# Kernel optimization log

Hardware: AMD Instinct MI355X
Metric: run time of the kernel (lower is better)

Reference implementation:

```python
import jax, jax.numpy as jnp
import numpy as np

TOP_K = 2
NUM_EXPERTS = 64
LOAD_BALANCE_ALPHA = 0.01
Z_LOSS_ALPHA = 1e-4
TEMPERATURE = 1.0  # buffer init, clamped to [0.1, 2.0] -> 1.0 (seq_len < 8192 branch)


def setup_inputs() -> dict:
    key = jax.random.key(0)
    k1, k2 = jax.random.split(key)
    x = jax.random.normal(k1, (4, 4096, 1024), dtype=jnp.float32)
    gate_w = jax.random.normal(k2, (NUM_EXPERTS, 1024), dtype=jnp.float32) * (1.0 / np.sqrt(1024))
    return {"x": x, "gate_w": gate_w}


def reference(x, gate_w):
    B, S, H = x.shape
    x_flat = x.reshape(-1, H)                      # [T, H], T = B*S
    logits = jnp.einsum('th,eh->te', x_flat, gate_w)  # [T, E]
    logits = logits / TEMPERATURE
    scores = jax.nn.softmax(logits, axis=-1)       # [T, E]
    # eval path: dynamic_top_k == top_k, no noise / capacity limitation
    top_scores, top_idx = jax.lax.top_k(scores, TOP_K)   # [T, K]
    top_scores = jax.nn.softmax(top_scores.astype(jnp.float32), axis=-1).astype(x.dtype)
    # load-balance loss: squared deviation of mean expert load from uniform
    expert_load = scores.mean(axis=0)              # [E]
    ideal = 1.0 / NUM_EXPERTS
    lb_loss = LOAD_BALANCE_ALPHA * NUM_EXPERTS * jnp.sum((expert_load - ideal) ** 2)
    # z-loss: mean squared logsumexp of gate logits
    z = jax.nn.logsumexp(logits, axis=-1)          # [T]
    z_loss = Z_LOSS_ALPHA * jnp.mean(z ** 2)
    total_loss = lb_loss + z_loss
    return top_scores, top_idx, total_loss
```

## Files before the change

kernel.cpp:

```cpp
#include <hip/hip_runtime.h>
#include <math.h>

#define T_TOK 16384
#define NEXP  64


__global__ void moe_prep(const float* __restrict__ gw, float* __restrict__ ws) {
    __shared__ float tile[64][65];
    const int b = blockIdx.x;
    const int tid = threadIdx.x;
    if (b == 0 && tid < 128) ws[tid] = 0.f;
#pragma unroll
    for (int it = 0; it < 16; ++it) {
        int idx = it * 256 + tid;
        int e = idx >> 6, kk = idx & 63;
        tile[e][kk] = gw[e * 1024 + b * 64 + kk];
    }
    __syncthreads();
#pragma unroll
    for (int it = 0; it < 16; ++it) {
        int idx = it * 256 + tid;
        int kk = idx >> 6, e = idx & 63;
        ws[128 + (b * 64 + kk) * 64 + e] = tile[e][kk];
    }
}

__device__ __forceinline__ void pstore(float* B, const float (&a)[8][8],
                                       int tg, int eg) {
#pragma unroll
    for (int i = 0; i < 8; ++i) {
        float* p = B + (tg + 8 * i) * 68 + (eg << 3);
        *(float4*)(p)     = make_float4(a[i][0], a[i][1], a[i][2], a[i][3]);
        *(float4*)(p + 4) = make_float4(a[i][4], a[i][5], a[i][6], a[i][7]);
    }
}
__device__ __forceinline__ void padd(float* B, const float (&a)[8][8],
                                     int tg, int eg) {
#pragma unroll
    for (int i = 0; i < 8; ++i) {
        float* p = B + (tg + 8 * i) * 68 + (eg << 3);
        float4 v0 = *(float4*)(p);
        float4 v1 = *(float4*)(p + 4);
        v0.x += a[i][0]; v0.y += a[i][1]; v0.z += a[i][2]; v0.w += a[i][3];
        v1.x += a[i][4]; v1.y += a[i][5]; v1.z += a[i][6]; v1.w += a[i][7];
        *(float4*)(p)     = v0;
        *(float4*)(p + 4) = v1;
    }
}

__launch_bounds__(1024, 4)
__global__ void moe_main(const float* __restrict__ x,
                         const float* __restrict__ wt,
                         float* __restrict__ acc_ws,
                         float* __restrict__ out) {
    __shared__ float xbuf[64 * 68];
    __shared__ float wbuf[64 * 68];
    __shared__ float sc[64 * 68];
    __shared__ float row_inv[64];
    __shared__ float colpart[16][64];
    __shared__ int   is_last;

    const int tid  = threadIdx.x;
    const int lane = tid & 63;
    const int wv   = __builtin_amdgcn_readfirstlane(tid >> 6);
    const int tg   = lane & 7;
    const int eg   = lane >> 3;
    const int tok0 = blockIdx.x << 6;

    const int rr = tid >> 4;
    const int cg = tid & 15;
    const float* gx = x + (((size_t)(tok0 + rr)) << 10) + (cg << 2);
    const float* gw = wt + (rr << 6) + (cg << 2);
    const int lof = rr * 68 + (cg << 2);

    float acc[8][8];
#pragma unroll
    for (int i = 0; i < 8; ++i)
#pragma unroll
        for (int j = 0; j < 8; ++j) acc[i][j] = 0.f;

    const float* xr = xbuf + tg * 68 + (wv << 2);
    const float* wr = wbuf + (wv * 4) * 68 + (eg << 3);

    float4 px = *(const float4*)gx;
    float4 pw = *(const float4*)gw;

#pragma unroll 1
    for (int s = 0; s < 16; ++s) {
        __syncthreads();
        *(float4*)(xbuf + lof) = px;
        *(float4*)(wbuf + lof) = pw;
        __syncthreads();
        if (s < 15) {
            px = *(const float4*)(gx + ((s + 1) << 6));
            pw = *(const float4*)(gw + ((s + 1) << 12));
        }
        float wa[4][8];
#pragma unroll
        for (int u = 0; u < 4; ++u) {
            float4 q0 = *(const float4*)(wr + u * 68);
            float4 q1 = *(const float4*)(wr + u * 68 + 4);
            wa[u][0] = q0.x; wa[u][1] = q0.y; wa[u][2] = q0.z; wa[u][3] = q0.w;
            wa[u][4] = q1.x; wa[u][5] = q1.y; wa[u][6] = q1.z; wa[u][7] = q1.w;
        }
#pragma unroll
        for (int i = 0; i < 8; ++i) {
            float4 xc = *(const float4*)(xr + i * 544);
            float xa[4] = {xc.x, xc.y, xc.z, xc.w};
#pragma unroll
            for (int u = 0; u < 4; ++u) {
                float xv = xa[u];
#pragma unroll
                for (int j = 0; j < 8; ++j)
                    acc[i][j] = fmaf(xv, wa[u][j], acc[i][j]);
            }
        }
    }

    __syncthreads();
    if      (wv == 0) pstore(sc,   acc, tg, eg);
    else if (wv == 1) pstore(xbuf, acc, tg, eg);
    else if (wv == 2) pstore(wbuf, acc, tg, eg);
    __syncthreads();
    if      (wv == 3) padd(sc,   acc, tg, eg);
    else if (wv == 4) padd(xbuf, acc, tg, eg);
    else if (wv == 5) padd(wbuf, acc, tg, eg);
    __syncthreads();
    if      (wv == 6) padd(sc,   acc, tg, eg);
    else if (wv == 7) padd(xbuf, acc, tg, eg);
    else if (wv == 8) padd(wbuf, acc, tg, eg);
    __syncthreads();
    if      (wv == 9)  padd(sc,   acc, tg, eg);
    else if (wv == 10) padd(xbuf, acc, tg, eg);
    else if (wv == 11) padd(wbuf, acc, tg, eg);
    __syncthreads();
    if      (wv == 12) padd(sc,   acc, tg, eg);
    else if (wv == 13) padd(xbuf, acc, tg, eg);
    else if (wv == 14) padd(wbuf, acc, tg, eg);
    __syncthreads();
    if (wv == 15) padd(sc, acc, tg, eg);
    __syncthreads();
    {
        const int row = tid >> 4, g = tid & 15;
        float* ps = sc + row * 68 + (g << 2);
        float4 a  = *(float4*)ps;
        float4 bx = *(const float4*)(xbuf + row * 68 + (g << 2));
        float4 bw = *(const float4*)(wbuf + row * 68 + (g << 2));
        a.x += bx.x + bw.x; a.y += bx.y + bw.y;
        a.z += bx.z + bw.z; a.w += bx.w + bw.w;
        *(float4*)ps = a;
    }
    __syncthreads();

    if (tid < 64) {
        const int r = tid;
        const float* srow = sc + r * 68;
        float v1 = -1e30f, v2 = -1e30f;
        int i1 = 0, i2 = 0;
        for (int j = 0; j < 64; ++j) {
            float l = srow[j];
            if (l > v1)      { v2 = v1; i2 = i1; v1 = l; i1 = j; }
            else if (l > v2) { v2 = l; i2 = j; }
        }
        float m = v1;
        float ssum = 0.f;
        for (int j = 0; j < 64; ++j) {
            float ev = expf(srow[j] - m);
            ssum += ev;
            sc[r * 68 + j] = ev;
        }
        float inv = 1.f / ssum;
        row_inv[r] = inv;
        float z = m + logf(ssum);
        float zsq = z * z;
#pragma unroll
        for (int off = 32; off > 0; off >>= 1) zsq += __shfl_down(zsq, off);
        if (lane == 0) atomicAdd(acc_ws + 64, zsq);

        float p1s = inv;
        float p2s = expf(v2 - m) * inv;
        float bb  = expf(p2s - p1s);
        float s1 = 1.f / (1.f + bb);
        float s2 = bb * s1;
        int t = tok0 + r;
        out[2 * t]     = s1;
        out[2 * t + 1] = s2;
        out[2 * T_TOK + 2 * t]     = (float)i1;
        out[2 * T_TOK + 2 * t + 1] = (float)i2;
    }
    __syncthreads();

    {
        int e  = tid & 63;
        int rg = tid >> 6;
        float sum = 0.f;
#pragma unroll
        for (int r2 = 0; r2 < 4; ++r2) {
            int row = (rg << 2) + r2;
            sum += sc[row * 68 + e] * row_inv[row];
        }
        colpart[rg][e] = sum;
    }
    __syncthreads();
    if (tid < 64) {
        float tot = 0.f;
#pragma unroll
        for (int rg = 0; rg < 16; ++rg) tot += colpart[rg][tid];
        atomicAdd(acc_ws + tid, tot);
    }

    __syncthreads();
    if (tid == 0) {
        __threadfence();
        int old = __hip_atomic_fetch_add((int*)(acc_ws + 66), 1,
                                         __ATOMIC_ACQ_REL, __HIP_MEMORY_SCOPE_AGENT);
        is_last = (old == 255) ? 1 : 0;
    }
    __syncthreads();
    if (is_last && tid < 64) {
        __threadfence();
        float load = __hip_atomic_load(acc_ws + tid, __ATOMIC_RELAXED,
                                       __HIP_MEMORY_SCOPE_AGENT) * (1.f / 16384.f);
        float d = load - (1.f / 64.f);
        float v = d * d;
#pragma unroll
        for (int off = 32; off > 0; off >>= 1) v += __shfl_down(v, off);
        if (tid == 0) {
            float zsum = __hip_atomic_load(acc_ws + 64, __ATOMIC_RELAXED,
                                           __HIP_MEMORY_SCOPE_AGENT);
            float lb = 0.01f * 64.f * v;
            float zl = 1e-4f * zsum * (1.f / 16384.f);
            out[4 * T_TOK] = lb + zl;
        }
    }
}

extern "C" void kernel_launch(void* const* d_in, const int* in_sizes, int n_in,
                              void* d_out, int out_size, void* d_ws, size_t ws_size,
                              hipStream_t stream) {
    const float* x  = (const float*)d_in[0];
    const float* gw = (const float*)d_in[1];
    float* out = (float*)d_out;
    float* ws  = (float*)d_ws;

    moe_prep<<<16, 256, 0, stream>>>(gw, ws);
    moe_main<<<256, 1024, 0, stream>>>(x, ws + 128, ws, out);
}
```

Baseline: 131.0 us.

## Halve block to 512 threads with 8-wave K-split and two-stage reduction

Reduces moe_main to 512 threads (8 waves), so each wave covers 8 K-columns per 64-wide chunk instead of 4, loading two float4 per thread per stage. The inner product loop is reordered to load 8 x rows once and then stream w rows, and the cross-wave partial-sum reduction shrinks from 16 waves over 3 buffers to 8 waves over 2 buffers with fewer barriers. The aim is to cut reduction and sync overhead and shared-memory traffic per FMA. The cost is half the threads per block with launch bounds allowing only one block, which may lower latency hiding while streaming x from memory.

Result: no change. 128.5 us (-1.9%).

```diff
diff --git a/kernel.cpp b/kernel.cpp
--- a/kernel.cpp
+++ b/kernel.cpp
@@ -25,20 +25,20 @@
     }
 }
 
-__device__ __forceinline__ void pstore(float* B, const float (&a)[8][8],
-                                       int tg, int eg) {
+__device__ __forceinline__ void pst88(float* B, const float (&a)[8][8],
+                                      int ta, int eb) {
 #pragma unroll
     for (int i = 0; i < 8; ++i) {
-        float* p = B + (tg + 8 * i) * 68 + (eg << 3);
+        float* p = B + (ta + (i << 3)) * 68 + (eb << 3);
         *(float4*)(p)     = make_float4(a[i][0], a[i][1], a[i][2], a[i][3]);
         *(float4*)(p + 4) = make_float4(a[i][4], a[i][5], a[i][6], a[i][7]);
     }
 }
-__device__ __forceinline__ void padd(float* B, const float (&a)[8][8],
-                                     int tg, int eg) {
+__device__ __forceinline__ void pad88(float* B, const float (&a)[8][8],
+                                      int ta, int eb) {
 #pragma unroll
     for (int i = 0; i < 8; ++i) {
-        float* p = B + (tg + 8 * i) * 68 + (eg << 3);
+        float* p = B + (ta + (i << 3)) * 68 + (eb << 3);
         float4 v0 = *(float4*)(p);
         float4 v1 = *(float4*)(p + 4);
         v0.x += a[i][0]; v0.y += a[i][1]; v0.z += a[i][2]; v0.w += a[i][3];
@@ -48,7 +48,7 @@
     }
 }
 
-__launch_bounds__(1024, 4)
+__launch_bounds__(512, 1)
 __global__ void moe_main(const float* __restrict__ x,
                          const float* __restrict__ wt,
                          float* __restrict__ acc_ws,
@@ -56,22 +56,23 @@
     __shared__ float xbuf[64 * 68];
     __shared__ float wbuf[64 * 68];
     __shared__ float sc[64 * 68];
+    __shared__ float fb[64 * 68];
     __shared__ float row_inv[64];
-    __shared__ float colpart[16][64];
+    __shared__ float colpart[8][64];
     __shared__ int   is_last;
 
     const int tid  = threadIdx.x;
     const int lane = tid & 63;
     const int wv   = __builtin_amdgcn_readfirstlane(tid >> 6);
-    const int tg   = lane & 7;
-    const int eg   = lane >> 3;
+    const int ta   = lane >> 3;
+    const int eb   = lane & 7;
     const int tok0 = blockIdx.x << 6;
 
-    const int rr = tid >> 4;
-    const int cg = tid & 15;
-    const float* gx = x + (((size_t)(tok0 + rr)) << 10) + (cg << 2);
-    const float* gw = wt + (rr << 6) + (cg << 2);
-    const int lof = rr * 68 + (cg << 2);
+    const int rr  = tid >> 3;
+    const int sub = tid & 7;
+    const float* gx = x + (((size_t)(tok0 + rr)) << 10) + (sub << 2);
+    const float* gw = wt + (rr << 6) + (sub << 2);
+    const int slo = rr * 68 + (sub << 2);
 
     float acc[8][8];
 #pragma unroll
@@ -79,76 +80,76 @@
 #pragma unroll
         for (int j = 0; j < 8; ++j) acc[i][j] = 0.f;
 
-    const float* xr = xbuf + tg * 68 + (wv << 2);
-    const float* wr = wbuf + (wv * 4) * 68 + (eg << 3);
-
-    float4 px = *(const float4*)gx;
-    float4 pw = *(const float4*)gw;
+    float4 px0 = *(const float4*)(gx);
+    float4 px1 = *(const float4*)(gx + 32);
+    float4 pw0 = *(const float4*)(gw);
+    float4 pw1 = *(const float4*)(gw + 32);
 
 #pragma unroll 1
     for (int s = 0; s < 16; ++s) {
         __syncthreads();
-        *(float4*)(xbuf + lof) = px;
-        *(float4*)(wbuf + lof) = pw;
+        *(float4*)(xbuf + slo)      = px0;
+        *(float4*)(xbuf + slo + 32) = px1;
+        *(float4*)(wbuf + slo)      = pw0;
+        *(float4*)(wbuf + slo + 32) = pw1;
         __syncthreads();
         if (s < 15) {
-            px = *(const float4*)(gx + ((s + 1) << 6));
-            pw = *(const float4*)(gw + ((s + 1) << 12));
-        }
-        float wa[4][8];
-#pragma unroll
-        for (int u = 0; u < 4; ++u) {
-            float4 q0 = *(const float4*)(wr + u * 68);
-            float4 q1 = *(const float4*)(wr + u * 68 + 4);
-            wa[u][0] = q0.x; wa[u][1] = q0.y; wa[u][2] = q0.z; wa[u][3] = q0.w;
-            wa[u][4] = q1.x; wa[u][5] = q1.y; wa[u][6] = q1.z; wa[u][7] = q1.w;
-        }
-#pragma unroll
-        for (int i = 0; i < 8; ++i) {
-            float4 xc = *(const float4*)(xr + i * 544);
-            float xa[4] = {xc.x, xc.y, xc.z, xc.w};
+            px0 = *(const float4*)(gx + ((s + 1) << 6));
+            px1 = *(const float4*)(gx + ((s + 1) << 6) + 32);
+            pw0 = *(const float4*)(gw + ((s + 1) << 12));
+            pw1 = *(const float4*)(gw + ((s + 1) << 12) + 32);
+        }
+#pragma unroll
+        for (int cc = 0; cc < 2; ++cc) {
+            const int c4 = (wv << 3) + (cc << 2);
+            float xr[8][4];
+#pragma unroll
+            for (int i = 0; i < 8; ++i) {
+                float4 v = *(const float4*)(xbuf + (ta + (i << 3)) * 68 + c4);
+                xr[i][0] = v.x; xr[i][1] = v.y; xr[i][2] = v.z; xr[i][3] = v.w;
+            }
 #pragma unroll
             for (int u = 0; u < 4; ++u) {
-                float xv = xa[u];
-#pragma unroll
-                for (int j = 0; j < 8; ++j)
-                    acc[i][j] = fmaf(xv, wa[u][j], acc[i][j]);
+                const float* wr = wbuf + (c4 + u) * 68 + (eb << 3);
+                float4 w0 = *(const float4*)(wr);
+                float4 w1 = *(const float4*)(wr + 4);
+                float wa[8] = {w0.x, w0.y, w0.z, w0.w,
+                               w1.x, w1.y, w1.z, w1.w};
+#pragma unroll
+                for (int i = 0; i < 8; ++i) {
+                    const float xs = xr[i][u];
+#pragma unroll
+                    for (int j = 0; j < 8; ++j)
+                        acc[i][j] = fmaf(xs, wa[j], acc[i][j]);
+                }
             }
         }
     }
 
-    __syncthreads();
-    if      (wv == 0) pstore(sc,   acc, tg, eg);
-    else if (wv == 1) pstore(xbuf, acc, tg, eg);
-    else if (wv == 2) pstore(wbuf, acc, tg, eg);
-    __syncthreads();
-    if      (wv == 3) padd(sc,   acc, tg, eg);
-    else if (wv == 4) padd(xbuf, acc, tg, eg);
-    else if (wv == 5) padd(wbuf, acc, tg, eg);
-    __syncthreads();
-    if      (wv == 6) padd(sc,   acc, tg, eg);
-    else if (wv == 7) padd(xbuf, acc, tg, eg);
-    else if (wv == 8) padd(wbuf, acc, tg, eg);
-    __syncthreads();
-    if      (wv == 9)  padd(sc,   acc, tg, eg);
-    else if (wv == 10) padd(xbuf, acc, tg, eg);
-    else if (wv == 11) padd(wbuf, acc, tg, eg);
-    __syncthreads();
-    if      (wv == 12) padd(sc,   acc, tg, eg);
-    else if (wv == 13) padd(xbuf, acc, tg, eg);
-    else if (wv == 14) padd(wbuf, acc, tg, eg);
-    __syncthreads();
-    if (wv == 15) padd(sc, acc, tg, eg);
+    if      (wv == 0) pst88(sc, acc, ta, eb);
+    else if (wv == 1) pst88(fb, acc, ta, eb);
+    __syncthreads();
+    if      (wv == 2) pad88(sc, acc, ta, eb);
+    else if (wv == 3) pad88(fb, acc, ta, eb);
+    __syncthreads();
+    if      (wv == 4) pad88(sc, acc, ta, eb);
+    else if (wv == 5) pad88(fb, acc, ta, eb);
+    __syncthreads();
+    if      (wv == 6) pad88(sc, acc, ta, eb);
+    else if (wv == 7) pad88(fb, acc, ta, eb);
     __syncthreads();
     {
-        const int row = tid >> 4, g = tid & 15;
+        const int row = tid >> 3, g = tid & 7;
         float* ps = sc + row * 68 + (g << 2);
-        float4 a  = *(float4*)ps;
-        float4 bx = *(const float4*)(xbuf + row * 68 + (g << 2));
-        float4 bw = *(const float4*)(wbuf + row * 68 + (g << 2));
-        a.x += bx.x + bw.x; a.y += bx.y + bw.y;
-        a.z += bx.z + bw.z; a.w += bx.w + bw.w;
-        *(float4*)ps = a;
+        const float* pf = fb + row * 68 + (g << 2);
+        float4 a0 = *(float4*)(ps);
+        float4 b0 = *(const float4*)(pf);
+        a0.x += b0.x; a0.y += b0.y; a0.z += b0.z; a0.w += b0.w;
+        *(float4*)(ps) = a0;
+        float4 a1 = *(float4*)(ps + 32);
+        float4 b1 = *(const float4*)(pf + 32);
+        a1.x += b1.x; a1.y += b1.y; a1.z += b1.z; a1.w += b1.w;
+        *(float4*)(ps + 32) = a1;
     }
     __syncthreads();
 
@@ -195,8 +196,8 @@
         int rg = tid >> 6;
         float sum = 0.f;
 #pragma unroll
-        for (int r2 = 0; r2 < 4; ++r2) {
-            int row = (rg << 2) + r2;
+        for (int r2 = 0; r2 < 8; ++r2) {
+            int row = (rg << 3) + r2;
             sum += sc[row * 68 + e] * row_inv[row];
         }
         colpart[rg][e] = sum;
@@ -205,7 +206,7 @@
     if (tid < 64) {
         float tot = 0.f;
 #pragma unroll
-        for (int rg = 0; rg < 16; ++rg) tot += colpart[rg][tid];
+        for (int rg = 0; rg < 8; ++rg) tot += colpart[rg][tid];
         atomicAdd(acc_ws + tid, tot);
     }
 
@@ -244,5 +245,5 @@
     float* ws  = (float*)d_ws;
 
     moe_prep<<<16, 256, 0, stream>>>(gw, ws);
-    moe_main<<<256, 1024, 0, stream>>>(x, ws + 128, ws, out);
-}
+    moe_main<<<256, 512, 0, stream>>>(x, ws + 128, ws, out);
+}
```
